# Kernel optimization log

Measured on AMD Instinct MI355X. Metric: run time of the kernel, lower is better.

## Reference

```python
import jax, jax.numpy as jnp
import numpy as np

EMB_DIM = 1024
NUM_HEADS = 16
HEAD_DIM = EMB_DIM // NUM_HEADS


def _theta_vector(head_dim):
    # theta_i = 10000^(-2i/head_dim), i = 0..head_dim/2-1 (standard RoPE)
    i = jnp.arange(head_dim // 2, dtype=jnp.float32)
    return jnp.power(10000.0, -2.0 * i / head_dim)


def _apply_rope(x, cos, sin):
    # x: [B,S,H,D]; cos,sin: [B,S,1,D/2]. Pairwise 2x2 rotation per dim-pair.
    B, S, H, D = x.shape
    xp = x.reshape(B, S, H, D // 2, 2)
    x0, x1 = xp[..., 0], xp[..., 1]
    r0 = x0 * cos - x1 * sin
    r1 = x0 * sin + x1 * cos
    return jnp.stack([r0, r1], axis=-1).reshape(B, S, H, D)


def setup_inputs() -> dict:
    key = jax.random.key(0)
    ks = jax.random.split(key, 11)
    B, S = 2, 2048
    sc = 1.0 / np.sqrt(EMB_DIM)
    x = jax.random.normal(ks[0], (B, S, EMB_DIM), dtype=jnp.float32)
    positions = jnp.sort(jax.random.randint(ks[1], (B, S), 0, 8192), axis=-1)
    Wq = jax.random.normal(ks[2], (EMB_DIM, EMB_DIM), dtype=jnp.float32) * sc
    bq = jax.random.normal(ks[3], (EMB_DIM,), dtype=jnp.float32) * 0.01
    Wk = jax.random.normal(ks[4], (EMB_DIM, EMB_DIM), dtype=jnp.float32) * sc
    bk = jax.random.normal(ks[5], (EMB_DIM,), dtype=jnp.float32) * 0.01
    Wv = jax.random.normal(ks[6], (EMB_DIM, EMB_DIM), dtype=jnp.float32) * sc
    bv = jax.random.normal(ks[7], (EMB_DIM,), dtype=jnp.float32) * 0.01
    Wo = jax.random.normal(ks[8], (EMB_DIM, EMB_DIM), dtype=jnp.float32) * sc
    bo = jax.random.normal(ks[9], (EMB_DIM,), dtype=jnp.float32) * 0.01
    return {"x": x, "positions": positions, "Wq": Wq, "bq": bq, "Wk": Wk,
            "bk": bk, "Wv": Wv, "bv": bv, "Wo": Wo, "bo": bo}


def reference(x, positions, Wq, bq, Wk, bk, Wv, bv, Wo, bo):
    B, S, E = x.shape
    H, D = NUM_HEADS, HEAD_DIM
    Q = (x @ Wq + bq).reshape(B, S, H, D)
    K = (x @ Wk + bk).reshape(B, S, H, D)
    V = (x @ Wv + bv).reshape(B, S, H, D)
    theta = _theta_vector(D)                       # [D/2]
    ang = positions.astype(jnp.float32)[..., None] * theta  # [B,S,D/2]
    cos = jnp.cos(ang)[:, :, None, :]              # [B,S,1,D/2]
    sin = jnp.sin(ang)[:, :, None, :]
    Qr = _apply_rope(Q, cos, sin).transpose(0, 2, 1, 3)   # [B,H,S,D]
    Kr = _apply_rope(K, cos, sin).transpose(0, 2, 1, 3)
    Vh = V.transpose(0, 2, 1, 3)
    scores = jnp.einsum('bhqd,bhkd->bhqk', Qr, Kr) / jnp.sqrt(jnp.float32(D))
    probs = jax.nn.softmax(scores, axis=-1)
    ctx = jnp.einsum('bhqk,bhkd->bhqd', probs, Vh)
    ctx = ctx.transpose(0, 2, 1, 3).reshape(B, S, E)
    return ctx @ Wo + bo
```

## Files before the change

kernel.cpp:

```cpp
#include <hip/hip_runtime.h>
#include <hip/hip_bf16.h>
#include <math.h>

#define B_ 2
#define S_ 2048
#define E_ 1024
#define H_ 16
#define D_ 64
#define M_ 4096
#define NT2 32
#define KVB 64

typedef __bf16 bf16;
typedef __bf16 bf16x4 __attribute__((ext_vector_type(4)));
typedef __bf16 bf16x8 __attribute__((ext_vector_type(8)));
typedef float f32x4 __attribute__((ext_vector_type(4)));
typedef float f32x16 __attribute__((ext_vector_type(16)));

__device__ __forceinline__ void gload_lds16(const void* g, void* lds) {
  __builtin_amdgcn_global_load_lds(
      (const __attribute__((address_space(1))) unsigned int*)g,
      (__attribute__((address_space(3))) unsigned int*)lds, 16, 0, 0);
}

#define MFMA16(a, b, c) __builtin_amdgcn_mfma_f32_16x16x32_bf16(a, b, c, 0, 0, 0)
#define MFMA32(a, b, c) __builtin_amdgcn_mfma_f32_32x32x16_bf16(a, b, c, 0, 0, 0)
#define FENCE asm volatile("" ::: "memory")

__global__ __launch_bounds__(256)
void split_f32_kernel(const float* __restrict__ in, bf16* __restrict__ hi,
                      bf16* __restrict__ lo, int n4) {
  int i = blockIdx.x * 256 + threadIdx.x;
  if (i >= n4) return;
  float4 v = ((const float4*)in)[i];
  bf16 h0 = (bf16)v.x, h1 = (bf16)v.y, h2 = (bf16)v.z, h3 = (bf16)v.w;
  bf16x4 hv = {h0, h1, h2, h3};
  bf16x4 lv = {(bf16)(v.x - (float)h0), (bf16)(v.y - (float)h1),
               (bf16)(v.z - (float)h2), (bf16)(v.w - (float)h3)};
  *(bf16x4*)(hi + 4 * (size_t)i) = hv;
  *(bf16x4*)(lo + 4 * (size_t)i) = lv;
}

__global__ __launch_bounds__(256)
void transpose_split_kernel(const float* __restrict__ W, bf16* __restrict__ Th,
                            bf16* __restrict__ Tl) {
  __shared__ float tile[32][33];
  const int tx = threadIdx.x & 31, ty = threadIdx.x >> 5;
  const int c0 = blockIdx.x * 32, r0 = blockIdx.y * 32;
#pragma unroll
  for (int i = 0; i < 4; ++i)
    tile[ty + 8 * i][tx] = W[(size_t)(r0 + ty + 8 * i) * E_ + c0 + tx];
  __syncthreads();
#pragma unroll
  for (int i = 0; i < 4; ++i) {
    int rr = ty + 8 * i;
    float v = tile[tx][rr];
    bf16 hv = (bf16)v;
    size_t oidx = (size_t)(c0 + rr) * E_ + r0 + tx;
    Th[oidx] = hv;
    Tl[oidx] = (bf16)(v - (float)hv);
  }
}

__global__ __launch_bounds__(256)
void rope_tab_kernel(const int* __restrict__ pos, float* __restrict__ cosT,
                     float* __restrict__ sinT) {
  int idx = blockIdx.x * 256 + threadIdx.x;
  int t = idx & 31, bs = idx >> 5;
  double th = pow(10000.0, -(double)(2 * t) / 64.0);
  float ang = (float)pos[bs] * (float)th;
  double a = (double)ang;
  cosT[idx] = (float)cos(a);
  sinT[idx] = (float)sin(a);
}

#define BMq 256
#define BNq 256
#define BKq 32

__global__ __launch_bounds__(512, 2)
void gemm_qkv_kernel(const bf16* __restrict__ Ah_g, const bf16* __restrict__ Al_g,
                     const bf16* __restrict__ BhQ, const bf16* __restrict__ BlQ,
                     const bf16* __restrict__ BhK, const bf16* __restrict__ BlK,
                     const bf16* __restrict__ BhV, const bf16* __restrict__ BlV,
                     const float* __restrict__ bqp, const float* __restrict__ bkp,
                     const float* __restrict__ bvp,
                     const float* __restrict__ cosT, const float* __restrict__ sinT,
                     bf16* __restrict__ Qh, bf16* __restrict__ Qlo,
                     bf16* __restrict__ Kh, bf16* __restrict__ Klo,
                     bf16* __restrict__ VTb) {
  __shared__ bf16 lA_h[2][BMq * BKq], lA_l[2][BMq * BKq];
  __shared__ bf16 lB_h[2][BNq * BKq], lB_l[2][BNq * BKq];
  const int tid = threadIdx.x;
  const int lin = blockIdx.x;
  const int cc = (lin & 7) * 24 + (lin >> 3);
  const int third = cc >> 6;
  const int rem = cc & 63;
  const int n0 = (rem >> 4) * BNq;
  const int m0 = (rem & 15) * BMq;
  const bf16* Bh_g = third == 0 ? BhQ : third == 1 ? BhK : BhV;
  const bf16* Bl_g = third == 0 ? BlQ : third == 1 ? BlK : BlV;
  const float* bias = third == 0 ? bqp : third == 1 ? bkp : bvp;
  const int wave = tid >> 6, lane = tid & 63;
  const int wr = wave >> 2, wc = wave & 3;
  const int r = lane & 31, half = lane >> 5;
  const int KD = 1024;
  const int NK = KD / BKq;

  f32x16 acc[4][2] = {};

  auto stage = [&](int kt, int buf) {
    const int k0 = kt * BKq;
    const bf16* gsrc[4] = {Ah_g, Al_g, Bh_g, Bl_g};
    bf16* ldst[4] = {&lA_h[buf][0], &lA_l[buf][0], &lB_h[buf][0], &lB_l[buf][0]};
    const int rs[4] = {m0, m0, n0, n0};
#pragma unroll
    for (int mm = 0; mm < 4; ++mm) {
#pragma unroll
      for (int i = 0; i < 2; ++i) {
        int c = i * 512 + tid;
        int row = c >> 2, u = c & 3;
        int us = u ^ ((row >> 1) & 3);
        const char* gp =
            (const char*)(gsrc[mm] + (size_t)(rs[mm] + row) * KD + k0) + us * 16;
        char* lp = (char*)ldst[mm] + (size_t)(i * 512 + wave * 64) * 16;
        gload_lds16(gp, lp);
      }
    }
  };

  auto compute = [&](int buf) {
#pragma unroll
    for (int ks = 0; ks < 2; ++ks) {
      bf16x8 a_h[4], a_l[4], b_h[2], b_l[2];
#pragma unroll
      for (int mi = 0; mi < 4; ++mi) {
        int row = wr * 128 + mi * 32 + r;
        int boff = row * 64 + ((ks * 32 + half * 16) ^ (((row >> 1) & 3) << 4));
        a_h[mi] = *(const bf16x8*)((const char*)&lA_h[buf][0] + boff);
        a_l[mi] = *(const bf16x8*)((const char*)&lA_l[buf][0] + boff);
      }
#pragma unroll
      for (int ni = 0; ni < 2; ++ni) {
        int row = wc * 64 + ni * 32 + r;
        int boff = row * 64 + ((ks * 32 + half * 16) ^ (((row >> 1) & 3) << 4));
        b_h[ni] = *(const bf16x8*)((const char*)&lB_h[buf][0] + boff);
        b_l[ni] = *(const bf16x8*)((const char*)&lB_l[buf][0] + boff);
      }
#pragma unroll
      for (int mi = 0; mi < 4; ++mi)
#pragma unroll
        for (int ni = 0; ni < 2; ++ni) {
          acc[mi][ni] = MFMA32(a_h[mi], b_h[ni], acc[mi][ni]);
          acc[mi][ni] = MFMA32(a_h[mi], b_l[ni], acc[mi][ni]);
          acc[mi][ni] = MFMA32(a_l[mi], b_h[ni], acc[mi][ni]);
        }
    }
  };

  stage(0, 0);
  int cur = 0;
  for (int kt = 0; kt < NK - 1; ++kt) {
    stage(kt + 1, cur ^ 1);
    asm volatile("s_waitcnt vmcnt(8)" ::: "memory");
    __builtin_amdgcn_s_barrier();
    FENCE;
    compute(cur);
    FENCE;
    __builtin_amdgcn_s_barrier();
    FENCE;
    cur ^= 1;
  }
  asm volatile("s_waitcnt vmcnt(0)" ::: "memory");
  __builtin_amdgcn_s_barrier();
  FENCE;
  compute(cur);

#pragma unroll
  for (int mi = 0; mi < 4; ++mi)
#pragma unroll
    for (int ni = 0; ni < 2; ++ni) {
      const int gcol = n0 + wc * 64 + ni * 32 + r;
      const float bv = bias[gcol];
      if (third < 2) {
        bf16* outH = third == 0 ? Qh : Kh;
        bf16* outL = third == 0 ? Qlo : Klo;
        const int h = gcol >> 6, d = gcol & 63, tt = d >> 1;
#pragma unroll
        for (int tq = 0; tq < 4; ++tq) {
#pragma unroll
          for (int u = 0; u < 4; ++u) {
            int reg = tq * 4 + u;
            int grow = m0 + wr * 128 + mi * 32 + (u + 8 * tq + 4 * half);
            int s = grow & (S_ - 1), b = grow >> 11;
            float v = acc[mi][ni][reg] + bv;
            float other = __shfl_xor(v, 1);
            float cs = cosT[(size_t)(b * S_ + s) * NT2 + tt];
            float sn = sinT[(size_t)(b * S_ + s) * NT2 + tt];
            float vr = (d & 1) ? (other * sn + v * cs) : (v * cs - other * sn);
            if (third == 0) vr *= 0.125f;
            bf16 hv = (bf16)vr;
            bf16 lv = (bf16)(vr - (float)hv);
            size_t idx = (((size_t)(b * H_ + h)) * S_ + s) * D_ + d;
            outH[idx] = hv;
            outL[idx] = lv;
          }
        }
      } else {
        const int h = gcol >> 6, d = gcol & 63;
#pragma unroll
        for (int tq = 0; tq < 4; ++tq) {
          int grow = m0 + wr * 128 + mi * 32 + (8 * tq + 4 * half);
          int s = grow & (S_ - 1), b = grow >> 11;
          ushort4 pk;
          unsigned short* pp = (unsigned short*)&pk;
#pragma unroll
          for (int u = 0; u < 4; ++u) {
            float v = acc[mi][ni][tq * 4 + u] + bv;
            bf16 hv = (bf16)v;
            pp[u] = __builtin_bit_cast(unsigned short, hv);
          }
          *(ushort4*)((unsigned short*)VTb +
                      (((size_t)(b * H_ + h)) * D_ + d) * S_ + s) = pk;
        }
      }
    }
}

#define BMg 128
#define BNg 128
#define BKg 32

__global__ __launch_bounds__(256)
void gemm_o_kernel(const bf16* __restrict__ Ah_g, const bf16* __restrict__ Al_g,
                   const bf16* __restrict__ Bh_g, const bf16* __restrict__ Bl_g,
                   const float* __restrict__ bias, float* __restrict__ outF) {
  __shared__ bf16 lA_h[2][BMg * BKg], lA_l[2][BMg * BKg];
  __shared__ bf16 lB_h[2][BNg * BKg], lB_l[2][BNg * BKg];
  const int tid = threadIdx.x;
  const int lin = blockIdx.x;
  const int cc = (lin & 7) * 32 + (lin >> 3);
  const int nb = cc >> 5;
  const int mb = cc & 31;
  const int m0 = mb * BMg, n0 = nb * BNg;
  const int wave = tid >> 6, lane = tid & 63;
  const int wr = wave >> 1, wc = wave & 1;
  const int r = lane & 31, half = lane >> 5;
  const int KD = 1024;
  const int NK = KD / BKg;

  f32x16 acc[2][2] = {};

  auto stage = [&](int kt, int buf) {
    const int k0 = kt * BKg;
    const bf16* gsrc[4] = {Ah_g, Al_g, Bh_g, Bl_g};
    bf16* ldst[4] = {&lA_h[buf][0], &lA_l[buf][0], &lB_h[buf][0], &lB_l[buf][0]};
    const int rs[4] = {m0, m0, n0, n0};
#pragma unroll
    for (int mm = 0; mm < 4; ++mm) {
#pragma unroll
      for (int i = 0; i < 2; ++i) {
        int c = i * 256 + tid;
        int row = c >> 2, u = c & 3;
        int us = u ^ ((row >> 1) & 3);
        const char* gp =
            (const char*)(gsrc[mm] + (size_t)(rs[mm] + row) * KD + k0) + us * 16;
        char* lp = (char*)ldst[mm] + (size_t)(i * 256 + wave * 64) * 16;
        gload_lds16(gp, lp);
      }
    }
  };

  auto compute = [&](int buf) {
#pragma unroll
    for (int ks = 0; ks < 2; ++ks) {
      bf16x8 a_h[2], a_l[2], b_h[2], b_l[2];
#pragma unroll
      for (int mi = 0; mi < 2; ++mi) {
        int row = wr * 64 + mi * 32 + r;
        int boff = row * 64 + ((ks * 32 + half * 16) ^ (((row >> 1) & 3) << 4));
        a_h[mi] = *(const bf16x8*)((const char*)&lA_h[buf][0] + boff);
        a_l[mi] = *(const bf16x8*)((const char*)&lA_l[buf][0] + boff);
      }
#pragma unroll
      for (int ni = 0; ni < 2; ++ni) {
        int row = wc * 64 + ni * 32 + r;
        int boff = row * 64 + ((ks * 32 + half * 16) ^ (((row >> 1) & 3) << 4));
        b_h[ni] = *(const bf16x8*)((const char*)&lB_h[buf][0] + boff);
        b_l[ni] = *(const bf16x8*)((const char*)&lB_l[buf][0] + boff);
      }
#pragma unroll
      for (int mi = 0; mi < 2; ++mi)
#pragma unroll
        for (int ni = 0; ni < 2; ++ni) {
          acc[mi][ni] = MFMA32(a_h[mi], b_h[ni], acc[mi][ni]);
          acc[mi][ni] = MFMA32(a_h[mi], b_l[ni], acc[mi][ni]);
          acc[mi][ni] = MFMA32(a_l[mi], b_h[ni], acc[mi][ni]);
        }
    }
  };

  stage(0, 0);
  int cur = 0;
  for (int kt = 0; kt < NK - 1; ++kt) {
    stage(kt + 1, cur ^ 1);
    asm volatile("s_waitcnt vmcnt(8)" ::: "memory");
    __builtin_amdgcn_s_barrier();
    FENCE;
    compute(cur);
    FENCE;
    __builtin_amdgcn_s_barrier();
    FENCE;
    cur ^= 1;
  }
  asm volatile("s_waitcnt vmcnt(0)" ::: "memory");
  __builtin_amdgcn_s_barrier();
  FENCE;
  compute(cur);

#pragma unroll
  for (int mi = 0; mi < 2; ++mi)
#pragma unroll
    for (int ni = 0; ni < 2; ++ni) {
      const int gcol = n0 + wc * 64 + ni * 32 + r;
      const float bv = bias[gcol];
#pragma unroll
      for (int tq = 0; tq < 4; ++tq)
#pragma unroll
        for (int u = 0; u < 4; ++u) {
          int grow = m0 + wr * 64 + mi * 32 + (u + 8 * tq + 4 * half);
          outF[(size_t)grow * E_ + gcol] = acc[mi][ni][tq * 4 + u] + bv;
        }
    }
}

__global__ __launch_bounds__(256)
void attn_kernel(const bf16* __restrict__ Qh, const bf16* __restrict__ Ql,
                 const bf16* __restrict__ Kh, const bf16* __restrict__ Kl,
                 const bf16* __restrict__ VT, bf16* __restrict__ Ch,
                 bf16* __restrict__ Cl) {
  __shared__ bf16 sKh[2][KVB * 64];
  __shared__ bf16 sKl[2][KVB * 64];
  __shared__ bf16 sV[2][KVB * 64];

  const int tid = threadIdx.x;
  const int wave = tid >> 6, lane = tid & 63;
  const int r = lane & 15, hq = lane >> 4;
  const int bid = blockIdx.x;
  const int swz = (bid & 7) * 64 + (bid >> 3);
  const int bh = swz >> 4, qblk = swz & 15;
  const int q0 = qblk * 128 + wave * 32;
  const size_t hb = (size_t)bh * (S_ * D_);
  const size_t vb = (size_t)bh * (D_ * S_);

  bf16x8 qh[2][2], ql[2][2];
#pragma unroll
  for (int mi = 0; mi < 2; ++mi)
#pragma unroll
    for (int ks = 0; ks < 2; ++ks) {
      size_t off = hb + (size_t)(q0 + mi * 16 + r) * D_ + ks * 32 + hq * 8;
      qh[mi][ks] = *(const bf16x8*)&Qh[off];
      ql[mi][ks] = *(const bf16x8*)&Ql[off];
    }

  float m_lane[2] = {-1e30f, -1e30f};
  float l_lane[2] = {0.f, 0.f};
  f32x4 o[2][4] = {};

  auto stageK = [&](int kt, int buf) {
    const bf16* kbh = Kh + hb + (size_t)kt * (KVB * D_);
    const bf16* kbl = Kl + hb + (size_t)kt * (KVB * D_);
#pragma unroll
    for (int i = 0; i < 2; ++i) {
      int c = i * 256 + tid;
      int ldo = (i * 256 + wave * 64) * 16;
      int cs = c ^ ((c >> 3) & 7);
      gload_lds16(kbh + cs * 8, (char*)&sKh[buf][0] + ldo);
      gload_lds16(kbl + cs * 8, (char*)&sKl[buf][0] + ldo);
    }
  };
  uint4 vld[2];
  auto loadV = [&](int kt) {
    const bf16* vbp = VT + vb + kt * KVB;
#pragma unroll
    for (int i = 0; i < 2; ++i) {
      int c = i * 256 + tid;
      int row = c >> 3, w = c & 7;
      vld[i] = *(const uint4*)(vbp + (size_t)row * S_ + w * 8);
    }
  };
  auto writeV = [&](int buf) {
#pragma unroll
    for (int i = 0; i < 2; ++i) {
      int c = i * 256 + tid;
      int row = c >> 3, w = c & 7;
      int pb0 = (w >> 2) * 32 + (w & 1) * 16 + ((w >> 1) & 1) * 4;
      char* base = (char*)&sV[buf][0] + row * 128;
      uint2 lo = {vld[i].x, vld[i].y};
      uint2 hi = {vld[i].z, vld[i].w};
      *(uint2*)(base + ((pb0 * 2) ^ ((row & 7) << 4))) = lo;
      *(uint2*)(base + (((pb0 + 8) * 2) ^ ((row & 7) << 4))) = hi;
    }
  };

  stageK(0, 0);
  loadV(0);
  writeV(0);
  __syncthreads();
  int cur = 0;

  for (int kt = 0; kt < S_ / KVB; ++kt) {
    if (kt + 1 < S_ / KVB) {
      stageK(kt + 1, cur ^ 1);
      loadV(kt + 1);
    }

    f32x4 sf[2][4] = {};
#pragma unroll
    for (int nf = 0; nf < 4; ++nf)
#pragma unroll
      for (int ks = 0; ks < 2; ++ks) {
        int kk = nf * 16 + r;
        int boff = (kk * 128 + ks * 64 + hq * 16) ^ ((kk & 7) << 4);
        bf16x8 kkh = *(const bf16x8*)((const char*)&sKh[cur][0] + boff);
        bf16x8 kkl = *(const bf16x8*)((const char*)&sKl[cur][0] + boff);
#pragma unroll
        for (int mi = 0; mi < 2; ++mi) {
          sf[mi][nf] = MFMA16(kkh, qh[mi][ks], sf[mi][nf]);
          sf[mi][nf] = MFMA16(kkh, ql[mi][ks], sf[mi][nf]);
          sf[mi][nf] = MFMA16(kkl, qh[mi][ks], sf[mi][nf]);
        }
      }

    float lmax[2];
#pragma unroll
    for (int mi = 0; mi < 2; ++mi) {
      f32x4 m4;
#pragma unroll
      for (int e = 0; e < 4; ++e)
        m4[e] = fmaxf(fmaxf(sf[mi][0][e], sf[mi][1][e]),
                      fmaxf(sf[mi][2][e], sf[mi][3][e]));
      lmax[mi] = fmaxf(fmaxf(m4[0], m4[1]), fmaxf(m4[2], m4[3]));
    }
    int need = (lmax[0] > m_lane[0] + 8.f) || (lmax[1] > m_lane[1] + 8.f);
    if (__any(need)) {
#pragma unroll
      for (int mi = 0; mi < 2; ++mi) {
        float mx = lmax[mi];
        mx = fmaxf(mx, __shfl_xor(mx, 16));
        mx = fmaxf(mx, __shfl_xor(mx, 32));
        float mn = fmaxf(m_lane[mi], mx);
        float al = __expf(m_lane[mi] - mn);
        l_lane[mi] *= al;
        m_lane[mi] = mn;
        int alb = __builtin_bit_cast(int, al);
#pragma unroll
        for (int j = 0; j < 4; ++j) {
          int g = __builtin_amdgcn_ds_bpermute((hq * 4 + j) * 4, alb);
          float a = __builtin_bit_cast(float, g);
#pragma unroll
          for (int nd = 0; nd < 4; ++nd) o[mi][nd][j] *= a;
        }
      }
    }
    bf16x8 pa[2][2];
#pragma unroll
    for (int mi = 0; mi < 2; ++mi) {
      f32x4 s4 = {};
#pragma unroll
      for (int nf = 0; nf < 4; ++nf)
#pragma unroll
        for (int e = 0; e < 4; ++e) {
          float pv = __expf(sf[mi][nf][e] - m_lane[mi]);
          sf[mi][nf][e] = pv;
          s4[e] += pv;
        }
      l_lane[mi] += s4[0] + s4[1] + s4[2] + s4[3];
#pragma unroll
      for (int ks = 0; ks < 2; ++ks) {
        bf16x8 t;
#pragma unroll
        for (int e = 0; e < 4; ++e) {
          t[e] = (bf16)sf[mi][2 * ks][e];
          t[4 + e] = (bf16)sf[mi][2 * ks + 1][e];
        }
        pa[mi][ks] = t;
      }
    }

#pragma unroll
    for (int nd = 0; nd < 4; ++nd)
#pragma unroll
      for (int ks = 0; ks < 2; ++ks) {
        int dd = nd * 16 + r;
        int boff = (dd * 128 + ks * 64 + hq * 16) ^ ((dd & 7) << 4);
        bf16x8 vv = *(const bf16x8*)((const char*)&sV[cur][0] + boff);
#pragma unroll
        for (int mi = 0; mi < 2; ++mi)
          o[mi][nd] = MFMA16(pa[mi][ks], vv, o[mi][nd]);
      }

    if (kt + 1 < S_ / KVB) writeV(cur ^ 1);
    __syncthreads();
    cur ^= 1;
  }

  const int b = bh >> 4, h = bh & 15;
  float lq[2][4];
#pragma unroll
  for (int mi = 0; mi < 2; ++mi) {
    float lr = l_lane[mi];
    lr += __shfl_xor(lr, 16);
    lr += __shfl_xor(lr, 32);
    int lb = __builtin_bit_cast(int, lr);
#pragma unroll
    for (int j = 0; j < 4; ++j) {
      int g = __builtin_amdgcn_ds_bpermute((hq * 4 + j) * 4, lb);
      lq[mi][j] = __builtin_bit_cast(float, g);
    }
  }
#pragma unroll
  for (int mi = 0; mi < 2; ++mi)
#pragma unroll
    for (int nd = 0; nd < 4; ++nd)
#pragma unroll
      for (int j = 0; j < 4; ++j) {
        int s = q0 + mi * 16 + hq * 4 + j;
        int d = nd * 16 + r;
        float ov = o[mi][nd][j] / lq[mi][j];
        bf16 hv = (bf16)ov;
        bf16 lv = (bf16)(ov - (float)hv);
        size_t idx = (((size_t)(b * S_ + s)) * H_ + h) * D_ + d;
        Ch[idx] = hv;
        Cl[idx] = lv;
      }
}

extern "C" void kernel_launch(void* const* d_in, const int* in_sizes, int n_in,
                              void* d_out, int out_size, void* d_ws, size_t ws_size,
                              hipStream_t stream) {
  const float* x = (const float*)d_in[0];
  const int* pos = (const int*)d_in[1];
  const float* Wq = (const float*)d_in[2];
  const float* bq = (const float*)d_in[3];
  const float* Wk = (const float*)d_in[4];
  const float* bk = (const float*)d_in[5];
  const float* Wv = (const float*)d_in[6];
  const float* bv = (const float*)d_in[7];
  const float* Wo = (const float*)d_in[8];
  const float* bo = (const float*)d_in[9];
  float* out = (float*)d_out;

  char* p = (char*)d_ws;
  auto alloc = [&](size_t bytes) {
    char* rp = p;
    p += (bytes + 255) & ~(size_t)255;
    return rp;
  };
  const size_t XB = (size_t)M_ * E_ * sizeof(bf16);
  const size_t WB = (size_t)E_ * E_ * sizeof(bf16);
  const size_t TB = (size_t)B_ * S_ * NT2 * sizeof(float);
  bf16* Xh = (bf16*)alloc(XB);
  bf16* Xl = (bf16*)alloc(XB);
  bf16* WqTh = (bf16*)alloc(WB); bf16* WqTl = (bf16*)alloc(WB);
  bf16* WkTh = (bf16*)alloc(WB); bf16* WkTl = (bf16*)alloc(WB);
  bf16* WvTh = (bf16*)alloc(WB); bf16* WvTl = (bf16*)alloc(WB);
  bf16* WoTh = (bf16*)alloc(WB); bf16* WoTl = (bf16*)alloc(WB);
  float* cosT = (float*)alloc(TB);
  float* sinT = (float*)alloc(TB);
  bf16* Qh = (bf16*)alloc(XB); bf16* Qlo = (bf16*)alloc(XB);
  bf16* Kh = (bf16*)alloc(XB); bf16* Klo = (bf16*)alloc(XB);
  bf16* VTb = (bf16*)alloc(XB);
  bf16* Ch = Xh;
  bf16* Cl = Xl;

  split_f32_kernel<<<M_ * E_ / 4 / 256, 256, 0, stream>>>(x, Xh, Xl, M_ * E_ / 4);
  dim3 tg(32, 32);
  transpose_split_kernel<<<tg, 256, 0, stream>>>(Wq, WqTh, WqTl);
  transpose_split_kernel<<<tg, 256, 0, stream>>>(Wk, WkTh, WkTl);
  transpose_split_kernel<<<tg, 256, 0, stream>>>(Wv, WvTh, WvTl);
  transpose_split_kernel<<<tg, 256, 0, stream>>>(Wo, WoTh, WoTl);
  rope_tab_kernel<<<B_ * S_ * NT2 / 256, 256, 0, stream>>>(pos, cosT, sinT);

  gemm_qkv_kernel<<<192, 512, 0, stream>>>(Xh, Xl, WqTh, WqTl, WkTh, WkTl, WvTh,
                                           WvTl, bq, bk, bv, cosT, sinT, Qh, Qlo,
                                           Kh, Klo, VTb);

  attn_kernel<<<B_ * H_ * (S_ / 128), 256, 0, stream>>>(Qh, Qlo, Kh, Klo, VTb,
                                                        Ch, Cl);

  gemm_o_kernel<<<256, 256, 0, stream>>>(Ch, Cl, WoTh, WoTl, bo, out);
}
```

Measured before the change: 232.8 us.

## Interleave prefetch loads with MFMA compute and use one barrier per K-step

Restructures the QKV and output-projection GEMM main loops so the next tile's global-to-LDS loads are issued in chunks interleaved with the MFMA groups for each row block, instead of all at once before compute. It drops one of the two barriers per iteration, waits on all outstanding loads only at the end of the step, and raises wave priority around MFMA bursts with s_setprio. The aim is better overlap of memory traffic with matrix math and less sync overhead. Waiting for every load at the end of each step (vmcnt(0)) and removing the compiler memory fences could expose latency or let the compiler reorder LDS accesses across barriers.

```diff
diff --git a/kernel.cpp b/kernel.cpp
--- a/kernel.cpp
+++ b/kernel.cpp
@@ -25,7 +25,6 @@
 
 #define MFMA16(a, b, c) __builtin_amdgcn_mfma_f32_16x16x32_bf16(a, b, c, 0, 0, 0)
 #define MFMA32(a, b, c) __builtin_amdgcn_mfma_f32_32x32x16_bf16(a, b, c, 0, 0, 0)
-#define FENCE asm volatile("" ::: "memory")
 
 __global__ __launch_bounds__(256)
 void split_f32_kernel(const float* __restrict__ in, bf16* __restrict__ hi,
@@ -109,72 +108,72 @@
 
   f32x16 acc[4][2] = {};
 
-  auto stage = [&](int kt, int buf) {
+  auto stage_pair = [&](int kt, int buf, int mm) {
     const int k0 = kt * BKq;
-    const bf16* gsrc[4] = {Ah_g, Al_g, Bh_g, Bl_g};
-    bf16* ldst[4] = {&lA_h[buf][0], &lA_l[buf][0], &lB_h[buf][0], &lB_l[buf][0]};
-    const int rs[4] = {m0, m0, n0, n0};
-#pragma unroll
-    for (int mm = 0; mm < 4; ++mm) {
-#pragma unroll
-      for (int i = 0; i < 2; ++i) {
-        int c = i * 512 + tid;
-        int row = c >> 2, u = c & 3;
-        int us = u ^ ((row >> 1) & 3);
-        const char* gp =
-            (const char*)(gsrc[mm] + (size_t)(rs[mm] + row) * KD + k0) + us * 16;
-        char* lp = (char*)ldst[mm] + (size_t)(i * 512 + wave * 64) * 16;
-        gload_lds16(gp, lp);
-      }
+    const bf16* gs = mm == 0 ? Ah_g : mm == 1 ? Al_g : mm == 2 ? Bh_g : Bl_g;
+    bf16* ld = mm == 0 ? &lA_h[buf][0] : mm == 1 ? &lA_l[buf][0]
+             : mm == 2 ? &lB_h[buf][0] : &lB_l[buf][0];
+    const int rbase = mm < 2 ? m0 : n0;
+#pragma unroll
+    for (int i = 0; i < 2; ++i) {
+      int c = i * 512 + tid;
+      int row = c >> 2, u = c & 3;
+      int us = u ^ ((row >> 1) & 3);
+      const char* gp =
+          (const char*)(gs + (size_t)(rbase + row) * KD + k0) + us * 16;
+      char* lp = (char*)ld + (size_t)(i * 512 + wave * 64) * 16;
+      gload_lds16(gp, lp);
     }
   };
 
-  auto compute = [&](int buf) {
-#pragma unroll
-    for (int ks = 0; ks < 2; ++ks) {
-      bf16x8 a_h[4], a_l[4], b_h[2], b_l[2];
-#pragma unroll
-      for (int mi = 0; mi < 4; ++mi) {
-        int row = wr * 128 + mi * 32 + r;
-        int boff = row * 64 + ((ks * 32 + half * 16) ^ (((row >> 1) & 3) << 4));
-        a_h[mi] = *(const bf16x8*)((const char*)&lA_h[buf][0] + boff);
-        a_l[mi] = *(const bf16x8*)((const char*)&lA_l[buf][0] + boff);
-      }
-#pragma unroll
-      for (int ni = 0; ni < 2; ++ni) {
-        int row = wc * 64 + ni * 32 + r;
-        int boff = row * 64 + ((ks * 32 + half * 16) ^ (((row >> 1) & 3) << 4));
-        b_h[ni] = *(const bf16x8*)((const char*)&lB_h[buf][0] + boff);
-        b_l[ni] = *(const bf16x8*)((const char*)&lB_l[buf][0] + boff);
-      }
-#pragma unroll
-      for (int mi = 0; mi < 4; ++mi)
+#pragma unroll
+  for (int mm = 0; mm < 4; ++mm) stage_pair(0, 0, mm);
+  asm volatile("s_waitcnt vmcnt(0)" ::: "memory");
+  __builtin_amdgcn_s_barrier();
+
+  int cur = 0;
+  for (int kt = 0; kt < NK; ++kt) {
+    const bool pf = (kt + 1 < NK);
+    bf16x8 b_h[2][2], b_l[2][2];
+#pragma unroll
+    for (int p = 0; p < 4; ++p) {
+      if (pf) stage_pair(kt + 1, cur ^ 1, p);
+      if (p == 0) {
+#pragma unroll
+        for (int ni = 0; ni < 2; ++ni)
+#pragma unroll
+          for (int ks = 0; ks < 2; ++ks) {
+            int brow = wc * 64 + ni * 32 + r;
+            int boff =
+                brow * 64 + ((ks * 32 + half * 16) ^ (((brow >> 1) & 3) << 4));
+            b_h[ni][ks] = *(const bf16x8*)((const char*)&lB_h[cur][0] + boff);
+            b_l[ni][ks] = *(const bf16x8*)((const char*)&lB_l[cur][0] + boff);
+          }
+      }
+      bf16x8 a_h2[2], a_l2[2];
+      const int arow = wr * 128 + p * 32 + r;
+#pragma unroll
+      for (int ks = 0; ks < 2; ++ks) {
+        int aoff =
+            arow * 64 + ((ks * 32 + half * 16) ^ (((arow >> 1) & 3) << 4));
+        a_h2[ks] = *(const bf16x8*)((const char*)&lA_h[cur][0] + aoff);
+        a_l2[ks] = *(const bf16x8*)((const char*)&lA_l[cur][0] + aoff);
+      }
+      __builtin_amdgcn_s_setprio(1);
+#pragma unroll
+      for (int ks = 0; ks < 2; ++ks)
 #pragma unroll
         for (int ni = 0; ni < 2; ++ni) {
-          acc[mi][ni] = MFMA32(a_h[mi], b_h[ni], acc[mi][ni]);
-          acc[mi][ni] = MFMA32(a_h[mi], b_l[ni], acc[mi][ni]);
-          acc[mi][ni] = MFMA32(a_l[mi], b_h[ni], acc[mi][ni]);
-        }
-    }
-  };
-
-  stage(0, 0);
-  int cur = 0;
-  for (int kt = 0; kt < NK - 1; ++kt) {
-    stage(kt + 1, cur ^ 1);
-    asm volatile("s_waitcnt vmcnt(8)" ::: "memory");
+          acc[p][ni] = MFMA32(a_h2[ks], b_h[ni][ks], acc[p][ni]);
+          acc[p][ni] = MFMA32(a_h2[ks], b_l[ni][ks], acc[p][ni]);
+          acc[p][ni] = MFMA32(a_l2[ks], b_h[ni][ks], acc[p][ni]);
+        }
+      __builtin_amdgcn_s_setprio(0);
+    }
+    if (pf) asm volatile("s_waitcnt vmcnt(0)" ::: "memory");
     __builtin_amdgcn_s_barrier();
-    FENCE;
-    compute(cur);
-    FENCE;
-    __builtin_amdgcn_s_barrier();
-    FENCE;
     cur ^= 1;
   }
-  asm volatile("s_waitcnt vmcnt(0)" ::: "memory");
-  __builtin_amdgcn_s_barrier();
-  FENCE;
-  compute(cur);
 
 #pragma unroll
   for (int mi = 0; mi < 4; ++mi)
@@ -251,72 +250,76 @@
 
   f32x16 acc[2][2] = {};
 
-  auto stage = [&](int kt, int buf) {
+  auto stage_pair = [&](int kt, int buf, int p) {
     const int k0 = kt * BKg;
-    const bf16* gsrc[4] = {Ah_g, Al_g, Bh_g, Bl_g};
-    bf16* ldst[4] = {&lA_h[buf][0], &lA_l[buf][0], &lB_h[buf][0], &lB_l[buf][0]};
-    const int rs[4] = {m0, m0, n0, n0};
-#pragma unroll
-    for (int mm = 0; mm < 4; ++mm) {
+#pragma unroll
+    for (int j = 0; j < 2; ++j) {
+      int mm = p * 2 + j;
+      const bf16* gs = mm == 0 ? Ah_g : mm == 1 ? Al_g : mm == 2 ? Bh_g : Bl_g;
+      bf16* ld = mm == 0 ? &lA_h[buf][0] : mm == 1 ? &lA_l[buf][0]
+               : mm == 2 ? &lB_h[buf][0] : &lB_l[buf][0];
+      const int rbase = mm < 2 ? m0 : n0;
 #pragma unroll
       for (int i = 0; i < 2; ++i) {
         int c = i * 256 + tid;
         int row = c >> 2, u = c & 3;
         int us = u ^ ((row >> 1) & 3);
         const char* gp =
-            (const char*)(gsrc[mm] + (size_t)(rs[mm] + row) * KD + k0) + us * 16;
-        char* lp = (char*)ldst[mm] + (size_t)(i * 256 + wave * 64) * 16;
+            (const char*)(gs + (size_t)(rbase + row) * KD + k0) + us * 16;
+        char* lp = (char*)ld + (size_t)(i * 256 + wave * 64) * 16;
         gload_lds16(gp, lp);
       }
     }
   };
 
-  auto compute = [&](int buf) {
-#pragma unroll
-    for (int ks = 0; ks < 2; ++ks) {
-      bf16x8 a_h[2], a_l[2], b_h[2], b_l[2];
-#pragma unroll
-      for (int mi = 0; mi < 2; ++mi) {
-        int row = wr * 64 + mi * 32 + r;
-        int boff = row * 64 + ((ks * 32 + half * 16) ^ (((row >> 1) & 3) << 4));
-        a_h[mi] = *(const bf16x8*)((const char*)&lA_h[buf][0] + boff);
-        a_l[mi] = *(const bf16x8*)((const char*)&lA_l[buf][0] + boff);
-      }
-#pragma unroll
-      for (int ni = 0; ni < 2; ++ni) {
-        int row = wc * 64 + ni * 32 + r;
-        int boff = row * 64 + ((ks * 32 + half * 16) ^ (((row >> 1) & 3) << 4));
-        b_h[ni] = *(const bf16x8*)((const char*)&lB_h[buf][0] + boff);
-        b_l[ni] = *(const bf16x8*)((const char*)&lB_l[buf][0] + boff);
-      }
-#pragma unroll
-      for (int mi = 0; mi < 2; ++mi)
+#pragma unroll
+  for (int p = 0; p < 2; ++p) stage_pair(0, 0, p);
+  asm volatile("s_waitcnt vmcnt(0)" ::: "memory");
+  __builtin_amdgcn_s_barrier();
+
+  int cur = 0;
+  for (int kt = 0; kt < NK; ++kt) {
+    const bool pf = (kt + 1 < NK);
+    bf16x8 b_h[2][2], b_l[2][2];
+#pragma unroll
+    for (int p = 0; p < 2; ++p) {
+      if (pf) stage_pair(kt + 1, cur ^ 1, p);
+      if (p == 0) {
+#pragma unroll
+        for (int ni = 0; ni < 2; ++ni)
+#pragma unroll
+          for (int ks = 0; ks < 2; ++ks) {
+            int brow = wc * 64 + ni * 32 + r;
+            int boff =
+                brow * 64 + ((ks * 32 + half * 16) ^ (((brow >> 1) & 3) << 4));
+            b_h[ni][ks] = *(const bf16x8*)((const char*)&lB_h[cur][0] + boff);
+            b_l[ni][ks] = *(const bf16x8*)((const char*)&lB_l[cur][0] + boff);
+          }
+      }
+      bf16x8 a_h2[2], a_l2[2];
+      const int arow = wr * 64 + p * 32 + r;
+#pragma unroll
+      for (int ks = 0; ks < 2; ++ks) {
+        int aoff =
+            arow * 64 + ((ks * 32 + half * 16) ^ (((arow >> 1) & 3) << 4));
+        a_h2[ks] = *(const bf16x8*)((const char*)&lA_h[cur][0] + aoff);
+        a_l2[ks] = *(const bf16x8*)((const char*)&lA_l[cur][0] + aoff);
+      }
+      __builtin_amdgcn_s_setprio(1);
+#pragma unroll
+      for (int ks = 0; ks < 2; ++ks)
 #pragma unroll
         for (int ni = 0; ni < 2; ++ni) {
-          acc[mi][ni] = MFMA32(a_h[mi], b_h[ni], acc[mi][ni]);
-          acc[mi][ni] = MFMA32(a_h[mi], b_l[ni], acc[mi][ni]);
-          acc[mi][ni] = MFMA32(a_l[mi], b_h[ni], acc[mi][ni]);
-        }
-    }
-  };
-
-  stage(0, 0);
-  int cur = 0;
-  for (int kt = 0; kt < NK - 1; ++kt) {
-    stage(kt + 1, cur ^ 1);
-    asm volatile("s_waitcnt vmcnt(8)" ::: "memory");
+          acc[p][ni] = MFMA32(a_h2[ks], b_h[ni][ks], acc[p][ni]);
+          acc[p][ni] = MFMA32(a_h2[ks], b_l[ni][ks], acc[p][ni]);
+          acc[p][ni] = MFMA32(a_l2[ks], b_h[ni][ks], acc[p][ni]);
+        }
+      __builtin_amdgcn_s_setprio(0);
+    }
+    if (pf) asm volatile("s_waitcnt vmcnt(0)" ::: "memory");
     __builtin_amdgcn_s_barrier();
-    FENCE;
-    compute(cur);
-    FENCE;
-    __builtin_amdgcn_s_barrier();
-    FENCE;
     cur ^= 1;
   }
-  asm volatile("s_waitcnt vmcnt(0)" ::: "memory");
-  __builtin_amdgcn_s_barrier();
-  FENCE;
-  compute(cur);
 
 #pragma unroll
   for (int mi = 0; mi < 2; ++mi)
```

Measured after the change: 233.9 us. Within noise of the previous version (+0.5%).
